# Optimization experiments

Hardware: AMD Instinct MI355X
Metric: run time of the kernel (lower is better)

## Reference

```python
import jax, jax.numpy as jnp
import numpy as np

NUM_HEADS = 4
INITIAL_VALUE = 1.0
HEADS_RANGE = 3.0


def rotate_every_two(x):
    x1 = x[..., ::2]
    x2 = x[..., 1::2]
    return jnp.stack([-x2, x1], axis=-1).reshape(x.shape)


def theta_shift(x, sin, cos):
    return x * cos + rotate_every_two(x) * sin


def rel_pos_2d(h, w, key_dim):
    # angle: repeat each frequency twice -> length key_dim
    base = 1.0 / 10000.0 ** jnp.linspace(0.0, 1.0, key_dim // 2)
    angle = jnp.repeat(base, 2)
    decay = jnp.log(1.0 - 2.0 ** (-(INITIAL_VALUE + HEADS_RANGE * jnp.arange(NUM_HEADS, dtype=jnp.float32) / NUM_HEADS)))
    idx = jnp.arange(h * w, dtype=jnp.float32)
    sin = jnp.sin(idx[:, None] * angle[None, :]).reshape(h, w, key_dim)
    cos = jnp.cos(idx[:, None] * angle[None, :]).reshape(h, w, key_dim)
    def decay_1d(l):
        i = jnp.arange(l, dtype=jnp.float32)
        return jnp.abs(i[:, None] - i[None, :])[None, :, :] * decay[:, None, None]  # (n, l, l)
    return sin, cos, decay_1d(h), decay_1d(w)


def setup_inputs() -> dict:
    key = jax.random.key(0)
    b, C, H, W = 16, 256, 64, 64
    ks = jax.random.split(key, 12)
    gain = 2.0 ** (-2.5)
    xav = (2.0 / (C + C)) ** 0.5
    return {
        "x": jax.random.normal(ks[0], (b, C, H, W), jnp.float32),
        "Wq": jax.random.normal(ks[1], (C, C), jnp.float32) * gain * xav,
        "bq": jnp.zeros((C,), jnp.float32),
        "Wk": jax.random.normal(ks[2], (C, C), jnp.float32) * gain * xav,
        "bk": jnp.zeros((C,), jnp.float32),
        "Wv": jax.random.normal(ks[3], (C, C), jnp.float32) * gain * xav,
        "bv": jnp.zeros((C,), jnp.float32),
        "dw_kernel": jax.random.normal(ks[4], (5, 5, 1, C), jnp.float32) * 0.05,
        "dw_bias": jnp.zeros((C,), jnp.float32),
        "Wo": jax.random.normal(ks[5], (C, C), jnp.float32) * xav,
        "bo": jnp.zeros((C,), jnp.float32),
    }


def reference(x, Wq, bq, Wk, bk, Wv, bv, dw_kernel, dw_bias, Wo, bo):
    x = jnp.transpose(x, (0, 2, 3, 1))  # (b, h, w, c)
    b, h, w, c = x.shape
    n = NUM_HEADS
    d = c // n  # key_dim == head_dim (value_factor=1)
    scaling = d ** (-0.5)

    sin, cos, mask_h, mask_w = rel_pos_2d(h, w, d)

    q = x @ Wq + bq
    k = (x @ Wk + bk) * scaling
    v = x @ Wv + bv  # (b, h, w, c)

    # depthwise 5x5 conv (lepe) on v, NHWC
    lepe = jax.lax.conv_general_dilated(
        v, dw_kernel, window_strides=(1, 1), padding=((2, 2), (2, 2)),
        dimension_numbers=("NHWC", "HWIO", "NHWC"), feature_group_count=c,
    ) + dw_bias

    q = q.reshape(b, h, w, n, d).transpose(0, 3, 1, 2, 4)  # (b, n, h, w, d)
    k = k.reshape(b, h, w, n, d).transpose(0, 3, 1, 2, 4)
    qr = theta_shift(q, sin, cos)  # sin/cos (h,w,d) broadcast
    kr = theta_shift(k, sin, cos)

    # width-axis attention: rows independent
    qr_w = qr.transpose(0, 2, 1, 3, 4)  # (b, h, n, w, d)
    kr_w = kr.transpose(0, 2, 1, 3, 4)
    v5 = v.reshape(b, h, w, n, d).transpose(0, 1, 3, 2, 4)  # (b, h, n, w, d)
    qk_w = jnp.einsum("bhnqd,bhnkd->bhnqk", qr_w, kr_w) + mask_w  # (b,h,n,w,w)
    v5 = jnp.einsum("bhnqk,bhnkd->bhnqd", jax.nn.softmax(qk_w, axis=-1), v5)

    # height-axis attention: columns independent
    qr_h = qr.transpose(0, 3, 1, 2, 4)  # (b, w, n, h, d)
    kr_h = kr.transpose(0, 3, 1, 2, 4)
    v6 = v5.transpose(0, 3, 2, 1, 4)  # (b, w, n, h, d)
    qk_h = jnp.einsum("bwnqd,bwnkd->bwnqk", qr_h, kr_h) + mask_h  # (b,w,n,h,h)
    out = jnp.einsum("bwnqk,bwnkd->bwnqd", jax.nn.softmax(qk_h, axis=-1), v6)

    out = out.transpose(0, 3, 1, 2, 4).reshape(b, h, w, c)  # (b,h,w,n*d)
    out = (out + lepe) @ Wo + bo
    return jnp.transpose(out, (0, 3, 1, 2))  # (b, c, h, w)
```

## Files before the change

### kernel.cpp

```cpp
#include <hip/hip_runtime.h>
#include <hip/hip_bf16.h>

typedef unsigned short u16;
typedef unsigned int   u32;
typedef __attribute__((ext_vector_type(8))) short bf16x8;
typedef __attribute__((ext_vector_type(4))) float f32x4;

__device__ __forceinline__ float bf2f(u16 u) {
    union { u32 i; float f; } x; x.i = ((u32)u) << 16; return x.f;
}
__device__ __forceinline__ u16 f2bf(float f) {
    union { float f; u32 i; } x; x.f = f;
    u32 i = x.i;
    u32 r = (i + 0x7fffu + ((i >> 16) & 1u)) >> 16;
    return (u16)r;
}

__global__ void k_tables(float2* __restrict__ csT) {
    int id = blockIdx.x * 256 + threadIdx.x;
    int t = id >> 5, i = id & 31;
    double ang = pow(10000.0, -(double)i / 31.0);
    double a = (double)t * ang;
    csT[id] = make_float2((float)cos(a), (float)sin(a));
}

__global__ __launch_bounds__(256) void k_prep_w(
    const float* __restrict__ Wq, const float* __restrict__ Wk,
    const float* __restrict__ Wv, const float* __restrict__ Wo,
    u16* __restrict__ WTq, u16* __restrict__ WTk,
    u16* __restrict__ WTv, u16* __restrict__ WoT)
{
    __shared__ float T[32][33];
    int z = blockIdx.z;
    const float* W = (z == 0) ? Wq : (z == 1) ? Wk : (z == 2) ? Wv : Wo;
    u16* WT        = (z == 0) ? WTq : (z == 1) ? WTk : (z == 2) ? WTv : WoT;
    int n0 = blockIdx.x * 32, k0 = blockIdx.y * 32;
    int tx = threadIdx.x & 31, ty = threadIdx.x >> 5;
#pragma unroll
    for (int i = 0; i < 4; i++)
        T[ty * 4 + i][tx] = W[(k0 + ty * 4 + i) * 256 + n0 + tx];
    __syncthreads();
#pragma unroll
    for (int i = 0; i < 4; i++)
        WT[(n0 + ty * 4 + i) * 256 + k0 + tx] = f2bf(T[tx][ty * 4 + i]);
}

__global__ __launch_bounds__(512, 1) void k_qkv_fused(
    const float* __restrict__ x, const u16* __restrict__ WTall,
    const float* __restrict__ bq, const float* __restrict__ bk,
    const float* __restrict__ bv,
    const float2* __restrict__ csT,
    u16* __restrict__ qr, u16* __restrict__ kr, u16* __restrict__ vO,
    u16* __restrict__ v5)
{
    __shared__ alignas(16) char smem[163840];
    u16* Alds = (u16*)smem;
    u16* BldsA[2] = { (u16*)(smem + 65536),
                      (u16*)(smem + 98304) };
    float2* SL = (float2*)(smem + 131072);

    const int tid = threadIdx.x;
    const int t0 = blockIdx.x * 128;
    const int br = tid >> 3, bc = tid & 7;

    bf16x8 breg[4];
#pragma unroll
    for (int p = 0; p < 4; ++p)
        breg[p] = *(const bf16x8*)(WTall + (size_t)(p * 64 + br) * 256 + bc * 8);

    {
        float* Bf = (float*)(smem + 65536);
        const int b0 = t0 >> 12, sb0 = t0 & 4095;
        const float* xb = x + ((size_t)b0 * 256) * 4096 + sb0;
#pragma unroll
        for (int ch = 0; ch < 2; ++ch) {
#pragma unroll
            for (int p = 0; p < 8; ++p) {
                int it = p * 512 + tid;
                int c = it >> 5, s4 = (it & 31) * 4;
                float4 v4 = *(const float4*)(xb + (size_t)(ch * 128 + c) * 4096 + s4);
                *(float4*)(Bf + c * 128 + s4) = v4;
            }
            __syncthreads();
#pragma unroll
            for (int p = 0; p < 4; ++p) {
                int it = p * 512 + tid;
                int tok = it & 127, ck = it >> 7;
                u16 tmp[8];
#pragma unroll
                for (int j = 0; j < 8; ++j)
                    tmp[j] = f2bf(Bf[(ck * 8 + j) * 128 + tok]);
                int gc = ch * 16 + ck;
                int gcs = (gc & 24) | ((gc & 7) ^ (tok & 7));
                *(bf16x8*)(Alds + tok * 256 + gcs * 8) = *(bf16x8*)tmp;
            }
            __syncthreads();
        }
    }

    {
        const int sb = t0 & 4095;
#pragma unroll
        for (int p = 0; p < 8; ++p) {
            int idx = p * 512 + tid;
            SL[idx] = csT[(size_t)sb * 32 + idx];
        }
    }

    const int lane = tid & 63, w = tid >> 6;
    const int wr = w >> 2, wc = w & 3;
    const int l15 = lane & 15, l4 = lane >> 4, l7 = lane & 7;

    f32x4 acc[4][4];

#pragma unroll
    for (int mat = 0; mat < 3; ++mat) {
#pragma unroll
        for (int mi = 0; mi < 4; ++mi)
#pragma unroll
            for (int ni = 0; ni < 4; ++ni) acc[mi][ni] = (f32x4)0.f;

#pragma unroll
        for (int ks = 0; ks < 4; ++ks) {
            const int s = mat * 4 + ks;
            u16* Bl = BldsA[s & 1];
#pragma unroll
            for (int p = 0; p < 4; ++p) {
                int r = p * 64 + br;
                *(bf16x8*)(Bl + r * 64 + (bc ^ (r & 7)) * 8) = breg[p];
            }
            __syncthreads();
            if (s < 11) {
                const int s2 = s + 1;
                const int mat2 = s2 >> 2, ks2 = s2 & 3;
#pragma unroll
                for (int p = 0; p < 4; ++p)
                    breg[p] = *(const bf16x8*)(WTall + (size_t)mat2 * 65536 +
                                (size_t)(p * 64 + br) * 256 + ks2 * 64 + bc * 8);
            }
#pragma unroll
            for (int kk = 0; kk < 2; ++kk) {
                bf16x8 af[4], bfr[4];
#pragma unroll
                for (int mi = 0; mi < 4; ++mi) {
                    int r = wr * 64 + mi * 16 + l15;
                    af[mi] = *(const bf16x8*)(Alds + r * 256 + (ks * 8 + ((kk * 4 + l4) ^ l7)) * 8);
                }
#pragma unroll
                for (int ni = 0; ni < 4; ++ni) {
                    int r = wc * 64 + ni * 16 + l15;
                    bfr[ni] = *(const bf16x8*)(Bl + r * 64 + ((kk * 4 + l4) ^ l7) * 8);
                }
#pragma unroll
                for (int mi = 0; mi < 4; ++mi)
#pragma unroll
                    for (int ni = 0; ni < 4; ++ni)
                        acc[mi][ni] = __builtin_amdgcn_mfma_f32_16x16x32_bf16(
                            af[mi], bfr[ni], acc[mi][ni], 0, 0, 0);
            }
        }

        const float* bias = (mat == 0) ? bq : (mat == 1) ? bk : bv;
        u16* out          = (mat == 0) ? qr : (mat == 1) ? kr : vO;
        const float kscale = (mat == 1) ? 0.125f : 1.0f;
        float bcol[4]; int ip[4];
#pragma unroll
        for (int ni = 0; ni < 4; ++ni) {
            bcol[ni] = bias[wc * 64 + ni * 16 + l15];
            ip[ni] = (ni * 16 + l15) >> 1;
        }
#pragma unroll
        for (int mi = 0; mi < 4; ++mi) {
#pragma unroll
            for (int rg = 0; rg < 4; ++rg) {
                const int sl = wr * 64 + mi * 16 + l4 * 4 + rg;
                size_t trow = (size_t)(t0 + sl) * 256;
#pragma unroll
                for (int ni = 0; ni < 4; ++ni) {
                    float val = (acc[mi][ni][rg] + bcol[ni]) * kscale;
                    float prt = __shfl_xor(val, 1);
                    float res, res2;
                    if (mat != 2) {
                        float2 cs = SL[sl * 32 + ip[ni]];
                        res  = fmaf(val, cs.x, -prt * cs.y);
                        res2 = fmaf(prt, cs.x,  val * cs.y);
                    } else {
                        res = val; res2 = prt;
                    }
                    if (!(lane & 1)) {
                        u32 pk;
                        asm("v_cvt_pk_bf16_f32 %0, %1, %2" : "=v"(pk) : "v"(res), "v"(res2));
                        int o = wc * 64 + ni * 16 + l15;
                        *(u32*)(out + trow + o) = pk;
                    }
                }
            }
        }
    }

    __syncthreads();
    u16* VTl = (u16*)smem + w * 4608;
    u16* PLl = (u16*)(smem + 73728) + w * 4608;

    {
        float bcv[4];
#pragma unroll
        for (int ni = 0; ni < 4; ++ni) bcv[ni] = bv[wc * 64 + ni * 16 + l15];
#pragma unroll
        for (int mi = 0; mi < 4; ++mi)
#pragma unroll
            for (int ni = 0; ni < 4; ++ni) {
                int d = ni * 16 + l15;
                int gs = (mi * 2 + (l4 >> 1)) ^ (d >> 3);
                float e0 = acc[mi][ni][0] + bcv[ni], e1 = acc[mi][ni][1] + bcv[ni];
                float e2 = acc[mi][ni][2] + bcv[ni], e3 = acc[mi][ni][3] + bcv[ni];
                u32 p0, p1;
                asm("v_cvt_pk_bf16_f32 %0, %1, %2" : "=v"(p0) : "v"(e0), "v"(e1));
                asm("v_cvt_pk_bf16_f32 %0, %1, %2" : "=v"(p1) : "v"(e2), "v"(e3));
                uint2 pp; pp.x = p0; pp.y = p1;
                *(uint2*)(VTl + d * 72 + gs * 8 + (l4 & 1) * 4) = pp;
            }
    }

    asm volatile("s_waitcnt vmcnt(0)" ::: "memory");
    const size_t qkb = (size_t)(t0 + wr * 64) * 256 + wc * 64;
    bf16x8 ka[4][2], qb[4][2];
#pragma unroll
    for (int t = 0; t < 4; ++t)
#pragma unroll
        for (int ks = 0; ks < 2; ++ks) {
            ka[t][ks] = *(const bf16x8*)(kr + qkb + (size_t)(t * 16 + l15) * 256 + ks * 32 + l4 * 8);
            qb[t][ks] = *(const bf16x8*)(qr + qkb + (size_t)(t * 16 + l15) * 256 + ks * 32 + l4 * 8);
        }

    f32x4 sacc[4][4];
#pragma unroll
    for (int kt = 0; kt < 4; ++kt)
#pragma unroll
        for (int qt = 0; qt < 4; ++qt) sacc[kt][qt] = (f32x4)0.f;
#pragma unroll
    for (int ks = 0; ks < 2; ++ks)
#pragma unroll
        for (int kt = 0; kt < 4; ++kt)
#pragma unroll
            for (int qt = 0; qt < 4; ++qt)
                sacc[kt][qt] = __builtin_amdgcn_mfma_f32_16x16x32_bf16(
                    ka[kt][ks], qb[qt][ks], sacc[kt][qt], 0, 0, 0);

    const float decay = logf(1.0f - exp2f(-(1.0f + 0.75f * (float)wc)));
#pragma unroll
    for (int qt = 0; qt < 4; ++qt) {
        const int qq = qt * 16 + l15;
        float lsum = 0.f;
#pragma unroll
        for (int kt = 0; kt < 4; ++kt) {
            const int kb = kt * 16 + l4 * 4;
#pragma unroll
            for (int rr = 0; rr < 4; ++rr) {
                float s = sacc[kt][qt][rr] + fabsf((float)(qq - kb - rr)) * decay;
                s = __expf(s);
                sacc[kt][qt][rr] = s;
                lsum += s;
            }
        }
        lsum += __shfl_xor(lsum, 16);
        lsum += __shfl_xor(lsum, 32);
        const float rinv = 1.0f / lsum;
#pragma unroll
        for (int kt = 0; kt < 4; ++kt) {
            float e0 = sacc[kt][qt][0] * rinv, e1 = sacc[kt][qt][1] * rinv;
            float e2 = sacc[kt][qt][2] * rinv, e3 = sacc[kt][qt][3] * rinv;
            u32 p0, p1;
            asm("v_cvt_pk_bf16_f32 %0, %1, %2" : "=v"(p0) : "v"(e0), "v"(e1));
            asm("v_cvt_pk_bf16_f32 %0, %1, %2" : "=v"(p1) : "v"(e2), "v"(e3));
            uint2 pp; pp.x = p0; pp.y = p1;
            *(uint2*)(PLl + (qt * 16 + l15) * 72 + kt * 16 + l4 * 4) = pp;
        }
    }

    __builtin_amdgcn_s_waitcnt(0xC07F);
    bf16x8 pa[4][2], vb[4][2];
#pragma unroll
    for (int qt = 0; qt < 4; ++qt)
#pragma unroll
        for (int ks = 0; ks < 2; ++ks)
            pa[qt][ks] = *(const bf16x8*)(PLl + (qt * 16 + l15) * 72 + ks * 32 + l4 * 8);
#pragma unroll
    for (int dt = 0; dt < 4; ++dt)
#pragma unroll
        for (int ks = 0; ks < 2; ++ks) {
            int d = dt * 16 + l15;
            int g = (ks * 4 + l4) ^ (d >> 3);
            vb[dt][ks] = *(const bf16x8*)(VTl + d * 72 + g * 8);
        }

    f32x4 oacc[4][4];
#pragma unroll
    for (int qt = 0; qt < 4; ++qt)
#pragma unroll
        for (int dt = 0; dt < 4; ++dt) oacc[qt][dt] = (f32x4)0.f;
#pragma unroll
    for (int ks = 0; ks < 2; ++ks)
#pragma unroll
        for (int qt = 0; qt < 4; ++qt)
#pragma unroll
            for (int dt = 0; dt < 4; ++dt)
                oacc[qt][dt] = __builtin_amdgcn_mfma_f32_16x16x32_bf16(
                    pa[qt][ks], vb[dt][ks], oacc[qt][dt], 0, 0, 0);

#pragma unroll
    for (int qt = 0; qt < 4; ++qt)
#pragma unroll
        for (int dt = 0; dt < 4; ++dt)
#pragma unroll
            for (int rr = 0; rr < 4; ++rr)
                PLl[(qt * 16 + l4 * 4 + rr) * 72 + dt * 16 + l15] = f2bf(oacc[qt][dt][rr]);
    __builtin_amdgcn_s_waitcnt(0xC07F);

    const int b0 = t0 >> 12;
    const int line = ((t0 & 4095) >> 6) + wr;
    size_t orow = ((size_t)((b0 * 64 + lane) * 4 + wc)) * 4096 + line * 64;
#pragma unroll
    for (int c = 0; c < 8; ++c)
        *(bf16x8*)(v5 + orow + c * 8) = *(const bf16x8*)(PLl + lane * 72 + c * 8);
}

__global__ __launch_bounds__(256) void k_lepe(
    const u16* __restrict__ v, const float* __restrict__ dwk,
    const float* __restrict__ dwb, u16* __restrict__ lepe)
{
    __shared__ u16 VhU[12 * 12 * 64];
    __shared__ float Kl[25][64];
    const int b = blockIdx.z, cg = blockIdx.y * 64;
    const int ty0 = (blockIdx.x >> 3) * 8, tx0 = (blockIdx.x & 7) * 8;
    const int tid = threadIdx.x;

    for (int idx = tid; idx < 1600; idx += 256) {
        int tap = idx >> 6, c = idx & 63;
        Kl[tap][c] = dwk[tap * 256 + cg + c];
    }
#pragma unroll
    for (int p = 0; p < 9; ++p) {
        int idx = p * 256 + tid;
        int ch = idx & 15, pos = idx >> 4;
        int py = pos / 12, px = pos - py * 12;
        int gy = ty0 + py - 2, gx = tx0 + px - 2;
        ushort4 val = make_ushort4(0, 0, 0, 0);
        if (gy >= 0 && gy < 64 && gx >= 0 && gx < 64)
            val = *(const ushort4*)(v + (size_t)(b * 4096 + gy * 64 + gx) * 256 + cg + ch * 4);
        *(ushort4*)(VhU + pos * 64 + ch * 4) = val;
    }
    __syncthreads();

    const int c = tid & 63, pg = tid >> 6;
    float kreg[25];
#pragma unroll
    for (int t = 0; t < 25; t++) kreg[t] = Kl[t][c];
    const float bias = dwb[cg + c];

    float acc[2][8];
#pragma unroll
    for (int t = 0; t < 2; ++t)
#pragma unroll
        for (int ox = 0; ox < 8; ++ox) acc[t][ox] = bias;

#pragma unroll
    for (int rr = 0; rr < 6; ++rr) {
        const int r = pg * 2 + rr;
        float rv[12];
#pragma unroll
        for (int px = 0; px < 12; ++px)
            rv[px] = bf2f(VhU[(r * 12 + px) * 64 + c]);
        if (rr <= 4) {
            const int dy = rr;
#pragma unroll
            for (int ox = 0; ox < 8; ++ox)
#pragma unroll
                for (int dx = 0; dx < 5; ++dx)
                    acc[0][ox] = fmaf(rv[ox + dx], kreg[dy * 5 + dx], acc[0][ox]);
        }
        if (rr >= 1) {
            const int dy = rr - 1;
#pragma unroll
            for (int ox = 0; ox < 8; ++ox)
#pragma unroll
                for (int dx = 0; dx < 5; ++dx)
                    acc[1][ox] = fmaf(rv[ox + dx], kreg[dy * 5 + dx], acc[1][ox]);
        }
    }

#pragma unroll
    for (int t = 0; t < 2; ++t) {
        const int oy = pg * 2 + t;
#pragma unroll
        for (int ox = 0; ox < 8; ++ox)
            lepe[(size_t)(b * 4096 + (ty0 + oy) * 64 + tx0 + ox) * 256 + cg + c] =
                f2bf(acc[t][ox]);
    }
}

__global__ __launch_bounds__(256) void k_attn_h(
    const u16* __restrict__ qr, const u16* __restrict__ kr,
    const u16* __restrict__ vsrc, const u16* __restrict__ lepeP,
    u16* __restrict__ outb)
{
    __shared__ u16 VT[4][64 * 72];
    __shared__ u16 PL[4][64 * 72];

    const int tid = threadIdx.x;
    const int w = tid >> 6, lane = tid & 63;
    const int l15 = lane & 15, l4 = lane >> 4;
    const int wid = blockIdx.x * 4 + w;
    const int b = wid >> 8, xy = (wid >> 2) & 63, n = wid & 3;

    const size_t qkbase = ((size_t)(b * 4096 + xy)) * 256 + n * 64;
    const int qkstride = 64 * 256;
    const size_t vbase = ((size_t)((b * 64 + xy) * 4 + n)) * 4096;
    const int vstride = 64;

    u16* VTl = &VT[w][0];
    u16* PLl = &PL[w][0];

    bf16x8 vld[8];
    const int vrow = lane >> 3, vchunk = lane & 7;
#pragma unroll
    for (int it = 0; it < 8; ++it)
        vld[it] = *(const bf16x8*)(vsrc + vbase + (size_t)(it * 8 + vrow) * vstride + vchunk * 8);

    bf16x8 ka[4][2], qb[4][2];
#pragma unroll
    for (int t = 0; t < 4; ++t)
#pragma unroll
        for (int ks = 0; ks < 2; ++ks) {
            ka[t][ks] = *(const bf16x8*)(kr + qkbase + (size_t)(t * 16 + l15) * qkstride + ks * 32 + l4 * 8);
            qb[t][ks] = *(const bf16x8*)(qr + qkbase + (size_t)(t * 16 + l15) * qkstride + ks * 32 + l4 * 8);
        }

    f32x4 sacc[4][4];
#pragma unroll
    for (int kt = 0; kt < 4; ++kt)
#pragma unroll
        for (int qt = 0; qt < 4; ++qt) sacc[kt][qt] = (f32x4)0.f;
#pragma unroll
    for (int ks = 0; ks < 2; ++ks)
#pragma unroll
        for (int kt = 0; kt < 4; ++kt)
#pragma unroll
            for (int qt = 0; qt < 4; ++qt)
                sacc[kt][qt] = __builtin_amdgcn_mfma_f32_16x16x32_bf16(
                    ka[kt][ks], qb[qt][ks], sacc[kt][qt], 0, 0, 0);

#pragma unroll
    for (int it = 0; it < 8; ++it) {
        int gp = ((it ^ vchunk) << 3) + vrow;
#pragma unroll
        for (int j = 0; j < 8; ++j) {
            int d = vchunk * 8 + j;
            VTl[d * 72 + gp] = (u16)vld[it][j];
        }
    }

    const float decay = logf(1.0f - exp2f(-(1.0f + 0.75f * (float)n)));
#pragma unroll
    for (int qt = 0; qt < 4; ++qt) {
        const int qq = qt * 16 + l15;
        float lsum = 0.f;
#pragma unroll
        for (int kt = 0; kt < 4; ++kt) {
            const int kb = kt * 16 + l4 * 4;
#pragma unroll
            for (int rr = 0; rr < 4; ++rr) {
                float s = sacc[kt][qt][rr] + fabsf((float)(qq - kb - rr)) * decay;
                s = __expf(s);
                sacc[kt][qt][rr] = s;
                lsum += s;
            }
        }
        lsum += __shfl_xor(lsum, 16);
        lsum += __shfl_xor(lsum, 32);
        const float rinv = 1.0f / lsum;
#pragma unroll
        for (int kt = 0; kt < 4; ++kt) {
            float e0 = sacc[kt][qt][0] * rinv, e1 = sacc[kt][qt][1] * rinv;
            float e2 = sacc[kt][qt][2] * rinv, e3 = sacc[kt][qt][3] * rinv;
            u32 p0, p1;
            asm("v_cvt_pk_bf16_f32 %0, %1, %2" : "=v"(p0) : "v"(e0), "v"(e1));
            asm("v_cvt_pk_bf16_f32 %0, %1, %2" : "=v"(p1) : "v"(e2), "v"(e3));
            uint2 pp; pp.x = p0; pp.y = p1;
            *(uint2*)(PLl + (qt * 16 + l15) * 72 + kt * 16 + l4 * 4) = pp;
        }
    }

    __builtin_amdgcn_s_waitcnt(0xC07F);
    bf16x8 pa[4][2], vb[4][2];
#pragma unroll
    for (int qt = 0; qt < 4; ++qt)
#pragma unroll
        for (int ks = 0; ks < 2; ++ks)
            pa[qt][ks] = *(const bf16x8*)(PLl + (qt * 16 + l15) * 72 + ks * 32 + l4 * 8);
#pragma unroll
    for (int dt = 0; dt < 4; ++dt)
#pragma unroll
        for (int ks = 0; ks < 2; ++ks) {
            int d = dt * 16 + l15;
            int g = (ks * 4 + l4) ^ (d >> 3);
            vb[dt][ks] = *(const bf16x8*)(VTl + d * 72 + g * 8);
        }

    f32x4 oacc[4][4];
#pragma unroll
    for (int qt = 0; qt < 4; ++qt)
#pragma unroll
        for (int dt = 0; dt < 4; ++dt) oacc[qt][dt] = (f32x4)0.f;
#pragma unroll
    for (int ks = 0; ks < 2; ++ks)
#pragma unroll
        for (int qt = 0; qt < 4; ++qt)
#pragma unroll
            for (int dt = 0; dt < 4; ++dt)
                oacc[qt][dt] = __builtin_amdgcn_mfma_f32_16x16x32_bf16(
                    pa[qt][ks], vb[dt][ks], oacc[qt][dt], 0, 0, 0);

#pragma unroll
    for (int qt = 0; qt < 4; ++qt)
#pragma unroll
        for (int dt = 0; dt < 4; ++dt)
#pragma unroll
            for (int rr = 0; rr < 4; ++rr)
                PLl[(qt * 16 + l4 * 4 + rr) * 72 + dt * 16 + l15] = f2bf(oacc[qt][dt][rr]);
    __builtin_amdgcn_s_waitcnt(0xC07F);

    size_t orow = ((size_t)(b * 4096 + lane * 64 + xy)) * 256 + n * 64;
#pragma unroll
    for (int c = 0; c < 8; ++c) {
        bf16x8 o8 = *(const bf16x8*)(PLl + lane * 72 + c * 8);
        bf16x8 lp = *(const bf16x8*)(lepeP + orow + c * 8);
        u16 hv[8];
#pragma unroll
        for (int j = 0; j < 8; ++j)
            hv[j] = f2bf(bf2f((u16)o8[j]) + bf2f((u16)lp[j]));
        *(bf16x8*)(outb + orow + c * 8) = *(bf16x8*)hv;
    }
}

__global__ __launch_bounds__(512, 1) void k_proj_fused(
    const u16* __restrict__ WoT, const u16* __restrict__ attnL,
    const float* __restrict__ bo, float* __restrict__ y)
{
    __shared__ alignas(16) u16 Alds[128 * 256];
    __shared__ alignas(16) u16 Blds[2][256 * 64];

    const int tid = threadIdx.x;
    const int bid = blockIdx.x;
    const int xcd = bid & 7, slot = bid >> 3;
    const int tt = xcd * 32 + (slot >> 1);
    const int oh = slot & 1;
    const int t0 = tt * 256;
    const int o0 = oh * 128;

    const int ar = tid >> 5, ac = tid & 31;
    const int br = tid >> 3, bc = tid & 7;

    bf16x8 breg[4];
    {
        bf16x8 areg[8];
#pragma unroll
        for (int p = 0; p < 8; ++p)
            areg[p] = *(const bf16x8*)(WoT + (size_t)(o0 + p * 16 + ar) * 256 + ac * 8);
#pragma unroll
        for (int p = 0; p < 4; ++p)
            breg[p] = *(const bf16x8*)(attnL + (size_t)(t0 + p * 64 + br) * 256 + bc * 8);
#pragma unroll
        for (int p = 0; p < 8; ++p) {
            int r = p * 16 + ar;
            *(bf16x8*)(Alds + r * 256 + (ac ^ (r & 7)) * 8) = areg[p];
        }
    }

    const int lane = tid & 63, w = tid >> 6;
    const int wr = w >> 2, wc = w & 3;
    const int l15 = lane & 15, l4 = lane >> 4, l7 = lane & 7;

    f32x4 acc[4][4];
#pragma unroll
    for (int mi = 0; mi < 4; ++mi)
#pragma unroll
        for (int ni = 0; ni < 4; ++ni) acc[mi][ni] = (f32x4)0.f;

#pragma unroll
    for (int ks = 0; ks < 4; ++ks) {
        u16* Bl = &Blds[ks & 1][0];
#pragma unroll
        for (int p = 0; p < 4; ++p) {
            int r = p * 64 + br;
            *(bf16x8*)(Bl + r * 64 + (bc ^ (r & 7)) * 8) = breg[p];
        }
        __syncthreads();
        if (ks < 3) {
#pragma unroll
            for (int p = 0; p < 4; ++p)
                breg[p] = *(const bf16x8*)(attnL + (size_t)(t0 + p * 64 + br) * 256 + (ks + 1) * 64 + bc * 8);
        }
#pragma unroll
        for (int kk = 0; kk < 2; ++kk) {
            bf16x8 af[4], bfr[4];
#pragma unroll
            for (int mi = 0; mi < 4; ++mi) {
                int r = wr * 64 + mi * 16 + l15;
                af[mi] = *(const bf16x8*)(Alds + r * 256 + (ks * 8 + ((kk * 4 + l4) ^ l7)) * 8);
            }
#pragma unroll
            for (int ni = 0; ni < 4; ++ni) {
                int r = wc * 64 + ni * 16 + l15;
                bfr[ni] = *(const bf16x8*)(Bl + r * 64 + ((kk * 4 + l4) ^ l7) * 8);
            }
#pragma unroll
            for (int mi = 0; mi < 4; ++mi)
#pragma unroll
                for (int ni = 0; ni < 4; ++ni)
                    acc[mi][ni] = __builtin_amdgcn_mfma_f32_16x16x32_bf16(
                        af[mi], bfr[ni], acc[mi][ni], 0, 0, 0);
        }
    }

    const int b = t0 >> 12, sb = t0 & 4095;
#pragma unroll
    for (int mi = 0; mi < 4; ++mi) {
#pragma unroll
        for (int rg = 0; rg < 4; ++rg) {
            int o = o0 + wr * 64 + mi * 16 + l4 * 4 + rg;
            float bb = bo[o];
            float* yrow = y + ((size_t)(b * 256 + o)) * 4096 + sb + wc * 64;
#pragma unroll
            for (int ni = 0; ni < 4; ++ni)
                yrow[ni * 16 + l15] = acc[mi][ni][rg] + bb;
        }
    }
}

extern "C" void kernel_launch(void* const* d_in, const int* in_sizes, int n_in,
                              void* d_out, int out_size, void* d_ws, size_t ws_size,
                              hipStream_t stream)
{
    const float* x   = (const float*)d_in[0];
    const float* Wq  = (const float*)d_in[1];
    const float* bq  = (const float*)d_in[2];
    const float* Wk  = (const float*)d_in[3];
    const float* bk  = (const float*)d_in[4];
    const float* Wv  = (const float*)d_in[5];
    const float* bv  = (const float*)d_in[6];
    const float* dwk = (const float*)d_in[7];
    const float* dwb = (const float*)d_in[8];
    const float* Wo  = (const float*)d_in[9];
    const float* bo  = (const float*)d_in[10];
    float* y = (float*)d_out;

    char* ws = (char*)d_ws;
    const size_t MB = 1024 * 1024;
    float2* csT = (float2*)(ws);
    u16* WTq = (u16*)(ws + 1 * MB);
    u16* WTk = WTq + 65536;
    u16* WTv = WTk + 65536;
    u16* WoT = WTv + 65536;
    u16* qr   = (u16*)(ws + 2 * MB);
    u16* kr   = (u16*)(ws + 2 * MB + 32 * MB);
    u16* v    = (u16*)(ws + 2 * MB + 64 * MB);
    u16* lepe = (u16*)(ws + 2 * MB + 96 * MB);
    u16* v5   = (u16*)(ws + 2 * MB + 128 * MB);
    u16* attn = v;

    k_tables<<<dim3(512), dim3(256), 0, stream>>>(csT);
    k_prep_w<<<dim3(8, 8, 4), dim3(256), 0, stream>>>(Wq, Wk, Wv, Wo, WTq, WTk, WTv, WoT);
    k_qkv_fused<<<dim3(512), dim3(512), 0, stream>>>(
        x, WTq, bq, bk, bv, csT, qr, kr, v, v5);
    k_lepe<<<dim3(64, 4, 16), dim3(256), 0, stream>>>(v, dwk, dwb, lepe);
    k_attn_h<<<dim3(1024), dim3(256), 0, stream>>>(qr, kr, v5, lepe, attn);
    k_proj_fused<<<dim3(512), dim3(512), 0, stream>>>(WoT, attn, bo, y);
}
```

Measured before the change: 195.0 us.

## Halve QKV block tile to 64 tokens to raise occupancy and drop LDS table

The fused QKV kernel now processes 64 tokens per block with 256 threads instead of 128 tokens with 512 threads. Shared memory falls from 160KB to 72KB so more blocks can be resident per CU. The K-loop uses 32-wide steps instead of 64-wide, with matching swizzle changes. The rotary cos/sin table is read straight from global memory instead of being staged in LDS. The trade-off is twice as many barriers per matrix, twice the weight traffic per token, and scattered global reads for the rotary table.

After: 221.5 us. 1.14x slower.

```diff
diff --git a/kernel.cpp b/kernel.cpp
--- a/kernel.cpp
+++ b/kernel.cpp
@@ -45,7 +45,7 @@
         WT[(n0 + ty * 4 + i) * 256 + k0 + tx] = f2bf(T[tx][ty * 4 + i]);
 }
 
-__global__ __launch_bounds__(512, 1) void k_qkv_fused(
+__global__ __launch_bounds__(256) void k_qkv_fused(
     const float* __restrict__ x, const u16* __restrict__ WTall,
     const float* __restrict__ bq, const float* __restrict__ bk,
     const float* __restrict__ bv,
@@ -53,15 +53,16 @@
     u16* __restrict__ qr, u16* __restrict__ kr, u16* __restrict__ vO,
     u16* __restrict__ v5)
 {
-    __shared__ alignas(16) char smem[163840];
+    __shared__ alignas(16) char smem[73728];
     u16* Alds = (u16*)smem;
-    u16* BldsA[2] = { (u16*)(smem + 65536),
-                      (u16*)(smem + 98304) };
-    float2* SL = (float2*)(smem + 131072);
+    u16* BldsA[2] = { (u16*)(smem + 32768),
+                      (u16*)(smem + 49152) };
 
     const int tid = threadIdx.x;
-    const int t0 = blockIdx.x * 128;
-    const int br = tid >> 3, bc = tid & 7;
+    const int t0 = blockIdx.x * 64;
+    const int sb = t0 & 4095;
+    const int b0 = t0 >> 12;
+    const int br = tid >> 2, bc = tid & 3;
 
     bf16x8 breg[4];
 #pragma unroll
@@ -69,27 +70,26 @@
         breg[p] = *(const bf16x8*)(WTall + (size_t)(p * 64 + br) * 256 + bc * 8);
 
     {
-        float* Bf = (float*)(smem + 65536);
-        const int b0 = t0 >> 12, sb0 = t0 & 4095;
-        const float* xb = x + ((size_t)b0 * 256) * 4096 + sb0;
+        float* Bf = (float*)(smem + 32768);
+        const float* xb = x + ((size_t)b0 * 256) * 4096 + sb;
 #pragma unroll
         for (int ch = 0; ch < 2; ++ch) {
 #pragma unroll
             for (int p = 0; p < 8; ++p) {
-                int it = p * 512 + tid;
-                int c = it >> 5, s4 = (it & 31) * 4;
+                int it = p * 256 + tid;
+                int c = it >> 4, s4 = (it & 15) * 4;
                 float4 v4 = *(const float4*)(xb + (size_t)(ch * 128 + c) * 4096 + s4);
-                *(float4*)(Bf + c * 128 + s4) = v4;
+                *(float4*)(Bf + c * 64 + s4) = v4;
             }
             __syncthreads();
 #pragma unroll
             for (int p = 0; p < 4; ++p) {
-                int it = p * 512 + tid;
-                int tok = it & 127, ck = it >> 7;
+                int it = p * 256 + tid;
+                int tok = it & 63, ck = it >> 6;
                 u16 tmp[8];
 #pragma unroll
                 for (int j = 0; j < 8; ++j)
-                    tmp[j] = f2bf(Bf[(ck * 8 + j) * 128 + tok]);
+                    tmp[j] = f2bf(Bf[(ck * 8 + j) * 64 + tok]);
                 int gc = ch * 16 + ck;
                 int gcs = (gc & 24) | ((gc & 7) ^ (tok & 7));
                 *(bf16x8*)(Alds + tok * 256 + gcs * 8) = *(bf16x8*)tmp;
@@ -98,17 +98,8 @@
         }
     }
 
-    {
-        const int sb = t0 & 4095;
-#pragma unroll
-        for (int p = 0; p < 8; ++p) {
-            int idx = p * 512 + tid;
-            SL[idx] = csT[(size_t)sb * 32 + idx];
-        }
-    }
-
     const int lane = tid & 63, w = tid >> 6;
-    const int wr = w >> 2, wc = w & 3;
+    const int wc = w;
     const int l15 = lane & 15, l4 = lane >> 4, l7 = lane & 7;
 
     f32x4 acc[4][4];
@@ -121,35 +112,36 @@
             for (int ni = 0; ni < 4; ++ni) acc[mi][ni] = (f32x4)0.f;
 
 #pragma unroll
-        for (int ks = 0; ks < 4; ++ks) {
-            const int s = mat * 4 + ks;
+        for (int ks = 0; ks < 8; ++ks) {
+            const int s = mat * 8 + ks;
             u16* Bl = BldsA[s & 1];
 #pragma unroll
             for (int p = 0; p < 4; ++p) {
                 int r = p * 64 + br;
-                *(bf16x8*)(Bl + r * 64 + (bc ^ (r & 7)) * 8) = breg[p];
+                *(bf16x8*)(Bl + r * 32 + (bc ^ (r & 3)) * 8) = breg[p];
             }
             __syncthreads();
-            if (s < 11) {
+            if (s < 23) {
                 const int s2 = s + 1;
-                const int mat2 = s2 >> 2, ks2 = s2 & 3;
+                const int mat2 = s2 >> 3, ks2 = s2 & 7;
 #pragma unroll
                 for (int p = 0; p < 4; ++p)
                     breg[p] = *(const bf16x8*)(WTall + (size_t)mat2 * 65536 +
-                                (size_t)(p * 64 + br) * 256 + ks2 * 64 + bc * 8);
-            }
-#pragma unroll
-            for (int kk = 0; kk < 2; ++kk) {
+                                (size_t)(p * 64 + br) * 256 + ks2 * 32 + bc * 8);
+            }
+            {
                 bf16x8 af[4], bfr[4];
+                const int gc = ks * 4 + l4;
+                const int gcs = (gc & 24) | ((gc & 7) ^ l7);
 #pragma unroll
                 for (int mi = 0; mi < 4; ++mi) {
-                    int r = wr * 64 + mi * 16 + l15;
-                    af[mi] = *(const bf16x8*)(Alds + r * 256 + (ks * 8 + ((kk * 4 + l4) ^ l7)) * 8);
+                    int r = mi * 16 + l15;
+                    af[mi] = *(const bf16x8*)(Alds + r * 256 + gcs * 8);
                 }
 #pragma unroll
                 for (int ni = 0; ni < 4; ++ni) {
                     int r = wc * 64 + ni * 16 + l15;
-                    bfr[ni] = *(const bf16x8*)(Bl + r * 64 + ((kk * 4 + l4) ^ l7) * 8);
+                    bfr[ni] = *(const bf16x8*)(Bl + r * 32 + (l4 ^ (r & 3)) * 8);
                 }
 #pragma unroll
                 for (int mi = 0; mi < 4; ++mi)
@@ -173,7 +165,7 @@
         for (int mi = 0; mi < 4; ++mi) {
 #pragma unroll
             for (int rg = 0; rg < 4; ++rg) {
-                const int sl = wr * 64 + mi * 16 + l4 * 4 + rg;
+                const int sl = mi * 16 + l4 * 4 + rg;
                 size_t trow = (size_t)(t0 + sl) * 256;
 #pragma unroll
                 for (int ni = 0; ni < 4; ++ni) {
@@ -181,7 +173,7 @@
                     float prt = __shfl_xor(val, 1);
                     float res, res2;
                     if (mat != 2) {
-                        float2 cs = SL[sl * 32 + ip[ni]];
+                        float2 cs = csT[(size_t)(sb + sl) * 32 + ip[ni]];
                         res  = fmaf(val, cs.x, -prt * cs.y);
                         res2 = fmaf(prt, cs.x,  val * cs.y);
                     } else {
@@ -200,7 +192,7 @@
 
     __syncthreads();
     u16* VTl = (u16*)smem + w * 4608;
-    u16* PLl = (u16*)(smem + 73728) + w * 4608;
+    u16* PLl = (u16*)(smem + 36864) + w * 4608;
 
     {
         float bcv[4];
@@ -223,7 +215,7 @@
     }
 
     asm volatile("s_waitcnt vmcnt(0)" ::: "memory");
-    const size_t qkb = (size_t)(t0 + wr * 64) * 256 + wc * 64;
+    const size_t qkb = (size_t)t0 * 256 + wc * 64;
     bf16x8 ka[4][2], qb[4][2];
 #pragma unroll
     for (int t = 0; t < 4; ++t)
@@ -317,8 +309,7 @@
                 PLl[(qt * 16 + l4 * 4 + rr) * 72 + dt * 16 + l15] = f2bf(oacc[qt][dt][rr]);
     __builtin_amdgcn_s_waitcnt(0xC07F);
 
-    const int b0 = t0 >> 12;
-    const int line = ((t0 & 4095) >> 6) + wr;
+    const int line = sb >> 6;
     size_t orow = ((size_t)((b0 * 64 + lane) * 4 + wc)) * 4096 + line * 64;
 #pragma unroll
     for (int c = 0; c < 8; ++c)
@@ -671,7 +662,7 @@
 
     k_tables<<<dim3(512), dim3(256), 0, stream>>>(csT);
     k_prep_w<<<dim3(8, 8, 4), dim3(256), 0, stream>>>(Wq, Wk, Wv, Wo, WTq, WTk, WTv, WoT);
-    k_qkv_fused<<<dim3(512), dim3(512), 0, stream>>>(
+    k_qkv_fused<<<dim3(1024), dim3(256), 0, stream>>>(
         x, WTq, bq, bk, bv, csT, qr, kr, v, v5);
     k_lepe<<<dim3(64, 4, 16), dim3(256), 0, stream>>>(v, dwk, dwb, lepe);
     k_attn_h<<<dim3(1024), dim3(256), 0, stream>>>(qr, kr, v5, lepe, attn);
```
